# Kernel tuning notes

Measured on AMD Instinct MI355X. Metric: run time of the kernel, lower is better.

## Reference

```python
import jax, jax.numpy as jnp
import numpy as np

N_E = 1024
E_DIM = 256
BETA = 0.25
PERSISTENCE = 0.1
B, T = 16, 1024


def setup_inputs() -> dict:
    key = jax.random.key(0)
    k1, k2 = jax.random.split(key)
    z = jax.random.normal(k1, (B, T, E_DIM), dtype=jnp.float32)
    # nn.Embedding(1+n_e, e_dim) init uniform(-1/n_e, 1/n_e)
    emb_weight = jax.random.uniform(k2, (N_E + 1, E_DIM), dtype=jnp.float32,
                                    minval=-1.0 / N_E, maxval=1.0 / N_E)
    return {"z": z, "emb_weight": emb_weight}


def _loss_contrast(z, ind, book):
    # z: (B,T,e), ind: (B,T) int, book: (n_e+1, e)
    z_q = book[ind]                                   # (B,T,e)
    loss_indices = jnp.sum((z - z_q) ** 2, axis=-1)   # (B,T)
    # ||z - book||^2 expanded to avoid the (B,T,n_e+1,e) intermediate
    z_sq = jnp.sum(z * z, axis=-1)                    # (B,T)
    b_sq = jnp.sum(book * book, axis=-1)              # (n_e+1,)
    cross = jnp.einsum('bte,ne->btn', z, book)        # (B,T,n_e+1)
    loss_all = z_sq[..., None] + b_sq[None, None, :] - 2.0 * cross
    lc = jnp.maximum(loss_indices[..., None] - loss_all + 1e-6 / N_E, 0.0)
    return jnp.mean(lc)


def _forward(z, emb_weight):
    zf = z.reshape(-1, E_DIM)
    d = (jnp.sum(zf * zf, axis=1, keepdims=True)
         + jnp.sum(emb_weight * emb_weight, axis=1)
         - 2.0 * (zf @ emb_weight.T)).reshape(B, T, N_E + 1)

    ind0 = jnp.clip(jnp.argmin(d[:, 0, :], axis=1), 0, N_E - 1)  # (B,)

    def step(carry, d_t):
        ind, coe = carry                              # (B,) int, (B,) f32
        d_here = jnp.take_along_axis(d_t, ind[:, None], axis=1)[:, 0]
        ind_next = jnp.minimum(ind + 1, N_E - 1)
        d_next = jnp.take_along_axis(d_t, ind_next[:, None], axis=1)[:, 0]
        stay = d_here <= d_next - coe
        ind_new = jnp.where(stay, ind, ind_next)
        coe_new = jnp.where(stay, coe + PERSISTENCE / N_E, 0.0)
        return (ind_new, coe_new), ind_new

    coe0 = jnp.zeros((B,), jnp.float32)
    _, inds = jax.lax.scan(step, (ind0, coe0), jnp.swapaxes(d[:, 1:, :], 0, 1))
    encoding_indices = jnp.concatenate([ind0[None, :], inds], axis=0).T  # (B,T)

    book_sg = jax.lax.stop_gradient(emb_weight)  # torch uses .data/.detach() everywhere
    z_q_raw = book_sg[encoding_indices]
    z_q = z + jax.lax.stop_gradient(z_q_raw - z)  # straight-through

    # non-legacy: beta * L(z, sg(book)) + L(sg(z), sg(book))
    loss = (BETA * _loss_contrast(z, encoding_indices, book_sg)
            + _loss_contrast(jax.lax.stop_gradient(z), encoding_indices, book_sg))

    v = jnp.max(encoding_indices) - jnp.min(encoding_indices)
    return z_q, loss, encoding_indices, v


def reference(z, emb_weight):
    return _forward(z, emb_weight)
```

## Files before the change

kernel.cpp:

```cpp
#include <hip/hip_runtime.h>

#define N_E   1024
#define EDIM  256
#define BB    16
#define TT    1024
#define NROW  (BB*TT)
#define NCOL  1025
#define NPAD  1152
#define PERS  (0.1f/1024.0f)
#define EPSC  (1e-6f/1024.0f)

#define OUT_LOSS 4194304
#define OUT_IDX  4194305
#define OUT_V    4210689

#define WS_ZB   0ull
#define WS_BBF  8388608ull
#define WS_BSQ  8978432ull
#define WS_E    8983552ull
#define WS_IND  84481024ull
#define WS_PART 84546560ull

typedef __attribute__((ext_vector_type(8))) short short8;
typedef __attribute__((ext_vector_type(4))) float floatx4;

__device__ __forceinline__ unsigned short f2bf(float f) {
    unsigned int u = __float_as_uint(f);
    u = (u + 0x7fffu + ((u >> 16) & 1u)) >> 16;
    return (unsigned short)u;
}

__device__ __forceinline__ float gload_f32(const float* p) {
    float r;
    asm volatile("global_load_dword %0, %1, off" : "=v"(r) : "v"(p));
    return r;
}

__global__ __launch_bounds__(256) void k0_prep(const float* __restrict__ z,
                                               const float* __restrict__ book,
                                               unsigned short* __restrict__ zb,
                                               unsigned short* __restrict__ bb,
                                               float* __restrict__ bsq) {
    int bx = blockIdx.x, tid = threadIdx.x;
    if (bx < 4096) {
        float4 v = ((const float4*)z)[bx * 256 + tid];
        size_t o = ((size_t)bx * 256 + tid) * 4;
        zb[o + 0] = f2bf(v.x); zb[o + 1] = f2bf(v.y);
        zb[o + 2] = f2bf(v.z); zb[o + 3] = f2bf(v.w);
    } else {
        int row = bx - 4096;
        float v = (row < NCOL) ? book[(size_t)row * EDIM + tid] : 0.0f;
        bb[(size_t)row * EDIM + tid] = f2bf(v);
        __shared__ float sd[256];
        sd[tid] = v * v;
        __syncthreads();
        for (int s = 128; s > 0; s >>= 1) { if (tid < s) sd[tid] += sd[tid + s]; __syncthreads(); }
        if (tid == 0) bsq[row] = sd[0];
    }
}

__global__ __launch_bounds__(256) void k1_gemm(const unsigned short* __restrict__ zb,
                                               const unsigned short* __restrict__ bb,
                                               const float* __restrict__ bsq,
                                               float* __restrict__ e) {
    int tid = threadIdx.x;
    int lane = tid & 63, w = tid >> 6;
    int mBase = blockIdx.x * 128 + (w >> 1) * 64;
    int nBase = blockIdx.y * 128 + (w & 1) * 64;
    int r = lane & 15, q = lane >> 4;

    floatx4 acc[4][4];
    #pragma unroll
    for (int i = 0; i < 4; i++)
        #pragma unroll
        for (int j = 0; j < 4; j++) acc[i][j] = (floatx4){0.f, 0.f, 0.f, 0.f};

    const short8* A = (const short8*)zb;
    const short8* Bm = (const short8*)bb;

    #pragma unroll
    for (int ks = 0; ks < 8; ks++) {
        int k8 = ks * 4 + q;
        short8 a[4], b[4];
        #pragma unroll
        for (int i = 0; i < 4; i++) a[i] = A[(size_t)(mBase + i * 16 + r) * 32 + k8];
        #pragma unroll
        for (int j = 0; j < 4; j++) b[j] = Bm[(size_t)(nBase + j * 16 + r) * 32 + k8];
        #pragma unroll
        for (int i = 0; i < 4; i++)
            #pragma unroll
            for (int j = 0; j < 4; j++)
                acc[i][j] = __builtin_amdgcn_mfma_f32_16x16x32_bf16(a[i], b[j], acc[i][j], 0, 0, 0);
    }

    float bsql[4];
    #pragma unroll
    for (int j = 0; j < 4; j++) bsql[j] = bsq[nBase + j * 16 + r];

    #pragma unroll
    for (int i = 0; i < 4; i++)
        #pragma unroll
        for (int rr = 0; rr < 4; rr++) {
            int m = mBase + i * 16 + q * 4 + rr;
            float* erow = e + (size_t)m * NPAD;
            #pragma unroll
            for (int j = 0; j < 4; j++)
                erow[nBase + j * 16 + r] = fmaf(-2.0f, acc[i][j][rr], bsql[j]);
        }
}


#define DECLW float A0_0, A0_1, A0_2, A0_3, A0_4, A1_0, A1_1, A1_2, A1_3, A1_4; \
              int q_0, q_1, q_2, q_3, q_4;

#define LDOP(S,k) { int _t = _tb + 2*k + _g; _t = _t < 1024 ? _t : 1023; \
                    A##S##_##k = gload_f32(_pe + (size_t)_t * NPAD); }
#define LDSET(S) LDOP(S,0) LDOP(S,1) LDOP(S,2) LDOP(S,3) LDOP(S,4)

#define QCOP(S,k) { float _bv = __shfl_down(A##S##_##k, 1, 32); \
                    int _qv = (int)((_bv - A##S##_##k) * QS); \
                    q_##k = _capn ? 0 : _qv; }
#define QCSET(S) QCOP(S,0) QCOP(S,1) QCOP(S,2) QCOP(S,3) QCOP(S,4)

#define CHS(j,k,h) { int _rel = ind - cbc; \
                     int _qv = __builtin_amdgcn_readlane(q_##k, _rel + h); \
                     bool _stay = (kk <= _qv); \
                     int _ip1 = ind + 1; _ip1 = _ip1 < 1023 ? _ip1 : 1023; \
                     ind = _stay ? ind : _ip1; \
                     kk  = _stay ? kk + 1 : 0; \
                     packed = (lane == j) ? ind : packed; }
#define CHAIN CHS(0,0,0) CHS(1,0,32) CHS(2,1,0) CHS(3,1,32) CHS(4,2,0) \
              CHS(5,2,32) CHS(6,3,0) CHS(7,3,32) CHS(8,4,0) CHS(9,4,32)

#define ITERX(SI, SQ) { \
    int cbI = ind < 992 ? ind : 992;                  \
    { const float* _pe = eb + cbI + _cl; int _tb = t + 20; LDSET(SI) } \
    __builtin_amdgcn_sched_barrier(0); \
    int packed = 0; \
    CHAIN \
    if (lane < 10 && t + lane < 1024) wind[ibase + t + lane] = packed; \
    __builtin_amdgcn_sched_barrier(0); \
    asm volatile("s_waitcnt vmcnt(6)" ::: "memory");  \
    __builtin_amdgcn_sched_barrier(0); \
    { bool _capn = (cbn + _cl == 1023); QCSET(SQ) } \
    cbc = cbn; cbn = cbI; \
    t += 10; }

__global__ __launch_bounds__(256, 1) void k2_scan(const float* __restrict__ z,
                                                  const float* __restrict__ book,
                                                  const float* __restrict__ bsq,
                                                  const float* __restrict__ e,
                                                  int* __restrict__ wind) {
    __shared__ float sb[4]; __shared__ int si[4];

    int b = blockIdx.x, tid = threadIdx.x;
    int lane = tid & 63, w = tid >> 6;

    const float4* zr = (const float4*)(z + (size_t)b * TT * EDIM);
    float4 zv = zr[lane];
    float s = zv.x * zv.x + zv.y * zv.y + zv.z * zv.z + zv.w * zv.w;
    #pragma unroll
    for (int off = 32; off; off >>= 1) s += __shfl_xor(s, off, 64);
    float zsq = s;

    float best = 3.4e38f; int bidx = 0;
    for (int wi = w; wi < 17; wi += 4) {
        int n = wi * 64 + lane;
        if (n < NCOL) {
            const float4* br = (const float4*)(book + (size_t)n * EDIM);
            float c0 = 0.f, c1 = 0.f, c2 = 0.f, c3 = 0.f;
            #pragma unroll 8
            for (int k = 0; k < 64; k++) {
                float4 bo = br[k]; float4 za = zr[k];
                c0 = fmaf(za.x, bo.x, c0); c1 = fmaf(za.y, bo.y, c1);
                c2 = fmaf(za.z, bo.z, c2); c3 = fmaf(za.w, bo.w, c3);
            }
            float cr = (c0 + c1) + (c2 + c3);
            float d0 = (zsq + bsq[n]) - 2.0f * cr;
            if (d0 < best || (d0 == best && n < bidx)) { best = d0; bidx = n; }
        }
    }
    #pragma unroll
    for (int off = 32; off; off >>= 1) {
        float ob = __shfl_xor(best, off, 64);
        int   oi = __shfl_xor(bidx, off, 64);
        if (ob < best || (ob == best && oi < bidx)) { best = ob; bidx = oi; }
    }
    if (lane == 0) { sb[w] = best; si[w] = bidx; }
    __syncthreads();
    if (w != 0) return;

    best = sb[0]; bidx = si[0];
    for (int i = 1; i < 4; i++) {
        float vv = sb[i]; int ii = si[i];
        if (vv < best || (vv == best && ii < bidx)) { best = vv; bidx = ii; }
    }

    int ind = min(bidx, N_E - 1);
    int kk = 0;
    size_t ibase = (size_t)b * TT;
    if (lane == 0) wind[ibase] = ind;

    const float* eb = e + (size_t)b * TT * NPAD;
    const float QS = 1.0f / PERS;

    int _g = lane >> 5;
    int _cl = lane & 31;

    DECLW

    int cbc = ind < 992 ? ind : 992;
    int cbn = cbc;
    { const float* _pe = eb + cbc + _cl; int _tb = 1;  LDSET(0) }
    { const float* _pe = eb + cbn + _cl; int _tb = 11; LDSET(1) }
    asm volatile("s_waitcnt vmcnt(5)" ::: "memory");
    __builtin_amdgcn_sched_barrier(0);
    { bool _capn = (cbc + _cl == 1023); QCSET(0) }

    int t = 1;
    #pragma unroll 1
    for (int cc = 0; cc < 52; cc++) {
        ITERX(0, 1)
        ITERX(1, 0)
    }
}

__global__ __launch_bounds__(256) void k3_loss_zq(const float* __restrict__ e,
                                                  const int* __restrict__ wind,
                                                  const float* __restrict__ book,
                                                  float* __restrict__ part,
                                                  float* __restrict__ out) {
    int rIdx = blockIdx.x, tid = threadIdx.x;
    int ind = wind[rIdx];
    const float* er = e + (size_t)rIdx * NPAD;
    float eind = er[ind];
    float p = 0.0f;
    for (int n = tid; n < NCOL; n += 256) {
        float v = eind - er[n] + EPSC;
        p += v > 0.0f ? v : 0.0f;
    }
    __shared__ float sd[256];
    sd[tid] = p; __syncthreads();
    for (int s = 128; s > 0; s >>= 1) { if (tid < s) sd[tid] += sd[tid + s]; __syncthreads(); }
    if (tid == 0) { part[rIdx] = sd[0]; out[OUT_IDX + rIdx] = (float)ind; }
    out[(size_t)rIdx * 256 + tid] = book[(size_t)ind * EDIM + tid];
}

__global__ __launch_bounds__(256) void k4_final(const float* __restrict__ part,
                                                const int* __restrict__ wind,
                                                float* __restrict__ out) {
    int tid = threadIdx.x;
    float s = 0.0f;
    for (int i = tid; i < NROW; i += 256) s += part[i];
    __shared__ float sd[256];
    sd[tid] = s; __syncthreads();
    for (int st = 128; st > 0; st >>= 1) { if (tid < st) sd[tid] += sd[tid + st]; __syncthreads(); }
    if (tid == 0) {
        int mn = wind[0], mx = wind[TT - 1];
        for (int b = 1; b < BB; b++) {
            mn = min(mn, wind[(size_t)b * TT]);
            mx = max(mx, wind[(size_t)b * TT + TT - 1]);
        }
        out[OUT_LOSS] = 1.25f * sd[0] / ((float)NROW * (float)NCOL);
        out[OUT_V] = (float)(mx - mn);
    }
}

extern "C" void kernel_launch(void* const* d_in, const int* in_sizes, int n_in,
                              void* d_out, int out_size, void* d_ws, size_t ws_size,
                              hipStream_t stream) {
    const float* z    = (const float*)d_in[0];
    const float* book = (const float*)d_in[1];
    char* ws = (char*)d_ws;
    unsigned short* zb = (unsigned short*)(ws + WS_ZB);
    unsigned short* bb = (unsigned short*)(ws + WS_BBF);
    float* bsq  = (float*)(ws + WS_BSQ);
    float* e    = (float*)(ws + WS_E);
    int*   wind = (int*)(ws + WS_IND);
    float* part = (float*)(ws + WS_PART);
    float* out  = (float*)d_out;

    hipLaunchKernelGGL(k0_prep,    dim3(4096 + 1152), dim3(256), 0, stream, z, book, zb, bb, bsq);
    hipLaunchKernelGGL(k1_gemm,    dim3(128, 9),      dim3(256), 0, stream, zb, bb, bsq, e);
    hipLaunchKernelGGL(k2_scan,    dim3(16),          dim3(256), 0, stream, z, book, bsq, e, wind);
    hipLaunchKernelGGL(k3_loss_zq, dim3(16384),       dim3(256), 0, stream, e, wind, book, part, out);
    hipLaunchKernelGGL(k4_final,   dim3(1),           dim3(256), 0, stream, part, wind, out);
}
```

Baseline: 241.0 us.

## Fuse loss and z_q gather into scan kernel with producer-consumer waves

Removes the separate per-row loss/gather kernel and folds its work into the sequential scan kernel. One wave runs the index chain and publishes chunk indices to LDS with a counter. Fifteen other waves poll that counter, then compute the hinge-loss partial sums and copy codebook rows for finished timesteps, overlapping with the latency-bound chain. The scan wave gets raised priority so it is not slowed by the consumers. The risk is that only 16 blocks do the loss work, so the memory bandwidth for reading the distance matrix may fall well short of the previous 16384-block launch.

```diff
diff --git a/kernel.cpp b/kernel.cpp
--- a/kernel.cpp
+++ b/kernel.cpp
@@ -109,6 +109,26 @@
         }
 }
 
+__device__ __forceinline__ float row_work(const float* er, int id, int lane,
+                                          const float4* book4, float4* out4,
+                                          float* out, size_t grow) {
+    float eind = er[id];
+    const float4* er4 = (const float4*)er;
+    float4 x0 = er4[lane], x1 = er4[lane + 64], x2 = er4[lane + 128], x3 = er4[lane + 192];
+    float e1024 = er[1024];
+    float p = 0.f;
+#define HG(v) { float _h = eind - (v) + EPSC; p += _h > 0.f ? _h : 0.f; }
+    HG(x0.x) HG(x0.y) HG(x0.z) HG(x0.w)
+    HG(x1.x) HG(x1.y) HG(x1.z) HG(x1.w)
+    HG(x2.x) HG(x2.y) HG(x2.z) HG(x2.w)
+    HG(x3.x) HG(x3.y) HG(x3.z) HG(x3.w)
+    if (lane == 0) { float _h = eind - e1024 + EPSC; p += _h > 0.f ? _h : 0.f; }
+#undef HG
+    out4[grow * 64 + lane] = book4[(size_t)id * 64 + lane];
+    if (lane == 0) out[OUT_IDX + grow] = (float)id;
+    return p;
+}
+
 
 #define DECLW float A0_0, A0_1, A0_2, A0_3, A0_4, A1_0, A1_1, A1_2, A1_3, A1_4; \
               int q_0, q_1, q_2, q_3, q_4;
@@ -137,8 +157,16 @@
     { const float* _pe = eb + cbI + _cl; int _tb = t + 20; LDSET(SI) } \
     __builtin_amdgcn_sched_barrier(0); \
     int packed = 0; \
+    __builtin_amdgcn_s_setprio(1); \
     CHAIN \
-    if (lane < 10 && t + lane < 1024) wind[ibase + t + lane] = packed; \
+    __builtin_amdgcn_s_setprio(0); \
+    if (lane < 10 && t + lane < 1024) { \
+        wind[ibase + t + lane] = packed; \
+        sind_lds[t + lane] = packed; \
+    } \
+    asm volatile("s_waitcnt lgkmcnt(0)" ::: "memory"); \
+    if (lane == 0) *(volatile int*)&done_cnt_s = cno + 1; \
+    cno++; \
     __builtin_amdgcn_sched_barrier(0); \
     asm volatile("s_waitcnt vmcnt(6)" ::: "memory");  \
     __builtin_amdgcn_sched_barrier(0); \
@@ -146,15 +174,23 @@
     cbc = cbn; cbn = cbI; \
     t += 10; }
 
-__global__ __launch_bounds__(256, 1) void k2_scan(const float* __restrict__ z,
-                                                  const float* __restrict__ book,
-                                                  const float* __restrict__ bsq,
-                                                  const float* __restrict__ e,
-                                                  int* __restrict__ wind) {
-    __shared__ float sb[4]; __shared__ int si[4];
+__global__ __launch_bounds__(1024, 1) void k2_scan(const float* __restrict__ z,
+                                                   const float* __restrict__ book,
+                                                   const float* __restrict__ bsq,
+                                                   const float* __restrict__ e,
+                                                   int* __restrict__ wind,
+                                                   float* __restrict__ part,
+                                                   float* __restrict__ out) {
+    __shared__ float sb[16]; __shared__ int si[16];
+    __shared__ int sind_lds[1024];
+    __shared__ int done_cnt_s;
+    __shared__ int ind0_s;
+    __shared__ float sd[1024];
 
     int b = blockIdx.x, tid = threadIdx.x;
     int lane = tid & 63, w = tid >> 6;
+
+    if (tid == 0) { done_cnt_s = 0; ind0_s = -1; }
 
     const float4* zr = (const float4*)(z + (size_t)b * TT * EDIM);
     float4 zv = zr[lane];
@@ -164,7 +200,7 @@
     float zsq = s;
 
     float best = 3.4e38f; int bidx = 0;
-    for (int wi = w; wi < 17; wi += 4) {
+    for (int wi = w; wi < 17; wi += 16) {
         int n = wi * 64 + lane;
         if (n < NCOL) {
             const float4* br = (const float4*)(book + (size_t)n * EDIM);
@@ -188,70 +224,82 @@
     }
     if (lane == 0) { sb[w] = best; si[w] = bidx; }
     __syncthreads();
-    if (w != 0) return;
-
-    best = sb[0]; bidx = si[0];
-    for (int i = 1; i < 4; i++) {
-        float vv = sb[i]; int ii = si[i];
-        if (vv < best || (vv == best && ii < bidx)) { best = vv; bidx = ii; }
-    }
-
-    int ind = min(bidx, N_E - 1);
-    int kk = 0;
-    size_t ibase = (size_t)b * TT;
-    if (lane == 0) wind[ibase] = ind;
-
-    const float* eb = e + (size_t)b * TT * NPAD;
-    const float QS = 1.0f / PERS;
-
-    int _g = lane >> 5;
-    int _cl = lane & 31;
-
-    DECLW
-
-    int cbc = ind < 992 ? ind : 992;
-    int cbn = cbc;
-    { const float* _pe = eb + cbc + _cl; int _tb = 1;  LDSET(0) }
-    { const float* _pe = eb + cbn + _cl; int _tb = 11; LDSET(1) }
-    asm volatile("s_waitcnt vmcnt(5)" ::: "memory");
-    __builtin_amdgcn_sched_barrier(0);
-    { bool _capn = (cbc + _cl == 1023); QCSET(0) }
-
-    int t = 1;
-    #pragma unroll 1
-    for (int cc = 0; cc < 52; cc++) {
-        ITERX(0, 1)
-        ITERX(1, 0)
-    }
-}
-
-__global__ __launch_bounds__(256) void k3_loss_zq(const float* __restrict__ e,
-                                                  const int* __restrict__ wind,
-                                                  const float* __restrict__ book,
-                                                  float* __restrict__ part,
-                                                  float* __restrict__ out) {
-    int rIdx = blockIdx.x, tid = threadIdx.x;
-    int ind = wind[rIdx];
-    const float* er = e + (size_t)rIdx * NPAD;
-    float eind = er[ind];
-    float p = 0.0f;
-    for (int n = tid; n < NCOL; n += 256) {
-        float v = eind - er[n] + EPSC;
-        p += v > 0.0f ? v : 0.0f;
-    }
-    __shared__ float sd[256];
-    sd[tid] = p; __syncthreads();
-    for (int s = 128; s > 0; s >>= 1) { if (tid < s) sd[tid] += sd[tid + s]; __syncthreads(); }
-    if (tid == 0) { part[rIdx] = sd[0]; out[OUT_IDX + rIdx] = (float)ind; }
-    out[(size_t)rIdx * 256 + tid] = book[(size_t)ind * EDIM + tid];
+
+    if (w != 0) {
+        const float* ebB = e + (size_t)b * TT * NPAD;
+        const float4* book4 = (const float4*)book;
+        float4* out4 = (float4*)out;
+        float psum = 0.f;
+        if (w == 1) {
+            while (*(volatile int*)&ind0_s < 0) __builtin_amdgcn_s_sleep(1);
+            int id0 = *(volatile int*)&ind0_s;
+            psum += row_work(ebB, id0, lane, book4, out4, out, (size_t)b * TT);
+        }
+        #pragma unroll 1
+        for (int c = w - 1; c <= 102; c += 15) {
+            while (*(volatile int*)&done_cnt_s < c + 1) __builtin_amdgcn_s_sleep(1);
+            int tb0 = 1 + 10 * c;
+            #pragma unroll 1
+            for (int jj = 0; jj < 10; jj++) {
+                int t = tb0 + jj;
+                if (t >= 1024) break;
+                int id = sind_lds[t];
+                psum += row_work(ebB + (size_t)t * NPAD, id, lane, book4, out4, out,
+                                 (size_t)b * TT + t);
+            }
+        }
+        sd[tid] = psum;
+    } else {
+        best = sb[0]; bidx = si[0];
+        for (int i = 1; i < 16; i++) {
+            float vv = sb[i]; int ii = si[i];
+            if (vv < best || (vv == best && ii < bidx)) { best = vv; bidx = ii; }
+        }
+
+        int ind = min(bidx, N_E - 1);
+        int kk = 0;
+        size_t ibase = (size_t)b * TT;
+        if (lane == 0) { wind[ibase] = ind; *(volatile int*)&ind0_s = ind; }
+
+        const float* eb = e + (size_t)b * TT * NPAD;
+        const float QS = 1.0f / PERS;
+
+        int _g = lane >> 5;
+        int _cl = lane & 31;
+        int cno = 0;
+
+        DECLW
+
+        int cbc = ind < 992 ? ind : 992;
+        int cbn = cbc;
+        { const float* _pe = eb + cbc + _cl; int _tb = 1;  LDSET(0) }
+        { const float* _pe = eb + cbn + _cl; int _tb = 11; LDSET(1) }
+        asm volatile("s_waitcnt vmcnt(5)" ::: "memory");
+        __builtin_amdgcn_sched_barrier(0);
+        { bool _capn = (cbc + _cl == 1023); QCSET(0) }
+
+        int t = 1;
+        #pragma unroll 1
+        for (int cc = 0; cc < 52; cc++) {
+            ITERX(0, 1)
+            ITERX(1, 0)
+        }
+        sd[tid] = 0.f;
+    }
+
+    __syncthreads();
+    for (int s2 = 512; s2 > 0; s2 >>= 1) {
+        if (tid < s2) sd[tid] += sd[tid + s2];
+        __syncthreads();
+    }
+    if (tid == 0) part[b] = sd[0];
 }
 
 __global__ __launch_bounds__(256) void k4_final(const float* __restrict__ part,
                                                 const int* __restrict__ wind,
                                                 float* __restrict__ out) {
     int tid = threadIdx.x;
-    float s = 0.0f;
-    for (int i = tid; i < NROW; i += 256) s += part[i];
+    float s = (tid < 16) ? part[tid] : 0.0f;
     __shared__ float sd[256];
     sd[tid] = s; __syncthreads();
     for (int st = 128; st > 0; st >>= 1) { if (tid < st) sd[tid] += sd[tid + st]; __syncthreads(); }
@@ -280,9 +328,8 @@
     float* part = (float*)(ws + WS_PART);
     float* out  = (float*)d_out;
 
-    hipLaunchKernelGGL(k0_prep,    dim3(4096 + 1152), dim3(256), 0, stream, z, book, zb, bb, bsq);
-    hipLaunchKernelGGL(k1_gemm,    dim3(128, 9),      dim3(256), 0, stream, zb, bb, bsq, e);
-    hipLaunchKernelGGL(k2_scan,    dim3(16),          dim3(256), 0, stream, z, book, bsq, e, wind);
-    hipLaunchKernelGGL(k3_loss_zq, dim3(16384),       dim3(256), 0, stream, e, wind, book, part, out);
-    hipLaunchKernelGGL(k4_final,   dim3(1),           dim3(256), 0, stream, part, wind, out);
-}
+    hipLaunchKernelGGL(k0_prep,  dim3(4096 + 1152), dim3(256),  0, stream, z, book, zb, bb, bsq);
+    hipLaunchKernelGGL(k1_gemm,  dim3(128, 9),      dim3(256),  0, stream, zb, bb, bsq, e);
+    hipLaunchKernelGGL(k2_scan,  dim3(16),          dim3(1024), 0, stream, z, book, bsq, e, wind, part, out);
+    hipLaunchKernelGGL(k4_final, dim3(1),           dim3(256),  0, stream, part, wind, out);
+}
```

After: 243.3 us. Within noise of the previous version (+1.0%).
